# Kernel optimization log

Measured on AMD Instinct MI355X. Metric: run time of the kernel, lower is better.

The kernel has to match this reference:

```python
import jax, jax.numpy as jnp
import numpy as np


def setup_inputs() -> dict:
    key = jax.random.key(0)
    k1, k2 = jax.random.split(key)
    B, T_src, H = 32, 1024, 512
    x = jax.random.normal(k1, (B, T_src, H), dtype=jnp.float32)
    durations = jax.random.randint(k2, (B, T_src), 0, 8, dtype=jnp.int32)
    return {"x": x, "durations": durations}


def reference(x, durations):
    """Length regulator: repeat each source frame x[b, s] durations[b, s] times,
    pad batch to the max expanded length, return (expanded, mel_masks) where
    mel_masks is True at padded positions. Vectorized via cumulative-duration
    searchsorted gather instead of per-batch repeat_interleave.
    x: (B, T_src, H) float, durations: (B, T_src) int.
    """
    B, T_src, H = x.shape
    cum = jnp.cumsum(durations.astype(jnp.int32), axis=1)      # (B, T_src)
    totals = cum[:, -1]                                        # (B,)
    max_len = int(jnp.max(totals))                             # static: concrete inputs
    t = jnp.arange(max_len, dtype=jnp.int32)                   # (T_mel,)
    # src index of output frame t: first s with cum[b, s] > t
    idx = jax.vmap(lambda c: jnp.searchsorted(c, t, side='right'))(cum)  # (B, T_mel)
    idx = jnp.clip(idx, 0, T_src - 1)
    out = jnp.take_along_axis(x, idx[..., None], axis=1)       # (B, T_mel, H)
    mel_masks = t[None, :] >= totals[:, None]                  # (B, T_mel) True = pad
    out = jnp.where(mel_masks[..., None], jnp.zeros((), dtype=x.dtype), out)
    return out, mel_masks
```

## Files before the change

### kernel.cpp

```cpp
#include <hip/hip_runtime.h>


#define B_SZ   32
#define T_SRC  1024
#define H_DIM  512

typedef float f4 __attribute__((ext_vector_type(4)));

__global__ void __launch_bounds__(T_SRC) lr_prep(const int* __restrict__ dur,
                                                 int* __restrict__ cum,
                                                 float* __restrict__ mask,
                                                 int max_len) {
    __shared__ int s[T_SRC];
    const int b   = blockIdx.x;
    const int tid = threadIdx.x;
    s[tid] = dur[b * T_SRC + tid];
    __syncthreads();
#pragma unroll
    for (int off = 1; off < T_SRC; off <<= 1) {
        int v = (tid >= off) ? s[tid - off] : 0;
        __syncthreads();
        s[tid] += v;
        __syncthreads();
    }
    cum[b * T_SRC + tid] = s[tid];
    const int total = s[T_SRC - 1];
    float* mb = mask + (size_t)b * max_len;
    for (int t = tid; t < max_len; t += T_SRC) mb[t] = (t < total) ? 0.0f : 1.0f;
}

__global__ void __launch_bounds__(256) lr_copy(const float* __restrict__ x,
                                               const int* __restrict__ cum,
                                               float* __restrict__ out,
                                               int max_len) {
    const int b    = blockIdx.y;
    const int lane = threadIdx.x & 63;
    const int s    = (blockIdx.x << 2) | (threadIdx.x >> 6);

    const int* cb = cum + b * T_SRC;

    const f4* src = (const f4*)(x + ((size_t)b * T_SRC + s) * H_DIM);
    const f4 v0 = src[lane];
    const f4 v1 = src[lane + 64];

    const int end   = cb[s];
    const int start = s ? cb[s - 1] : 0;

    float* ob = out + (size_t)b * max_len * H_DIM;
    for (int t = start; t < end; ++t) {
        f4* dst = (f4*)(ob + (size_t)t * H_DIM);
        __builtin_nontemporal_store(v0, dst + lane);
        __builtin_nontemporal_store(v1, dst + lane + 64);
    }

    const int total = cb[T_SRC - 1];
    const f4 z = (f4)(0.0f);
    for (int t = total + s; t < max_len; t += T_SRC) {
        f4* dst = (f4*)(ob + (size_t)t * H_DIM);
        __builtin_nontemporal_store(z, dst + lane);
        __builtin_nontemporal_store(z, dst + lane + 64);
    }
}

extern "C" void kernel_launch(void* const* d_in, const int* in_sizes, int n_in,
                              void* d_out, int out_size, void* d_ws, size_t ws_size,
                              hipStream_t stream) {
    const float* x   = (const float*)d_in[0];
    const int*   dur = (const int*)d_in[1];
    float*       out = (float*)d_out;
    int*         cumbuf = (int*)d_ws;

    const int max_len = out_size / (B_SZ * (H_DIM + 1));
    float* mask = out + (size_t)B_SZ * max_len * H_DIM;

    lr_prep<<<B_SZ, T_SRC, 0, stream>>>(dur, cumbuf, mask, max_len);

    dim3 grid(T_SRC / 4, B_SZ);
    lr_copy<<<grid, 256, 0, stream>>>(x, cumbuf, out, max_len);
}
```

Baseline: 293.0 us.

## Fuse cumsum prep into copy kernel with per-block wave-shuffle scan

```diff
diff --git a/kernel.cpp b/kernel.cpp
--- a/kernel.cpp
+++ b/kernel.cpp
@@ -4,61 +4,83 @@
 #define B_SZ   32
 #define T_SRC  1024
 #define H_DIM  512
+#define BLK_PER_B     64
+#define ROWS_PER_BLK  (T_SRC / BLK_PER_B)
+#define ROWS_PER_WAVE (ROWS_PER_BLK / 4)
 
 typedef float f4 __attribute__((ext_vector_type(4)));
+typedef int   i4 __attribute__((ext_vector_type(4)));
 
-__global__ void __launch_bounds__(T_SRC) lr_prep(const int* __restrict__ dur,
-                                                 int* __restrict__ cum,
-                                                 float* __restrict__ mask,
-                                                 int max_len) {
-    __shared__ int s[T_SRC];
-    const int b   = blockIdx.x;
-    const int tid = threadIdx.x;
-    s[tid] = dur[b * T_SRC + tid];
+__global__ void __launch_bounds__(256) lr_fused(const float* __restrict__ x,
+                                                const int* __restrict__ dur,
+                                                float* __restrict__ out,
+                                                float* __restrict__ mask,
+                                                int max_len) {
+    __shared__ int cumsh[T_SRC];
+    __shared__ int wsum[4];
+
+    const int b    = blockIdx.y;
+    const int bx   = blockIdx.x;
+    const int tid  = threadIdx.x;
+    const int lane = tid & 63;
+    const int wid  = tid >> 6;
+
+    const int r0 = bx * ROWS_PER_BLK + wid * ROWS_PER_WAVE;
+    const float* xb = x + (size_t)b * T_SRC * H_DIM;
+    f4 v0[ROWS_PER_WAVE], v1[ROWS_PER_WAVE];
+#pragma unroll
+    for (int i = 0; i < ROWS_PER_WAVE; ++i) {
+        const f4* src = (const f4*)(xb + (size_t)(r0 + i) * H_DIM);
+        v0[i] = src[lane];
+        v1[i] = src[lane + 64];
+    }
+
+    i4 d = ((const i4*)(dur + b * T_SRC))[tid];
+    const int s0 = d.x, s1 = s0 + d.y, s2 = s1 + d.z, s3 = s2 + d.w;
+    int v = s3;
+#pragma unroll
+    for (int off = 1; off < 64; off <<= 1) {
+        int u = __shfl_up(v, off);
+        if (lane >= off) v += u;
+    }
+    if (lane == 63) wsum[wid] = v;
     __syncthreads();
+    int wexcl = 0;
 #pragma unroll
-    for (int off = 1; off < T_SRC; off <<= 1) {
-        int v = (tid >= off) ? s[tid - off] : 0;
-        __syncthreads();
-        s[tid] += v;
-        __syncthreads();
-    }
-    cum[b * T_SRC + tid] = s[tid];
-    const int total = s[T_SRC - 1];
-    float* mb = mask + (size_t)b * max_len;
-    for (int t = tid; t < max_len; t += T_SRC) mb[t] = (t < total) ? 0.0f : 1.0f;
-}
-
-__global__ void __launch_bounds__(256) lr_copy(const float* __restrict__ x,
-                                               const int* __restrict__ cum,
-                                               float* __restrict__ out,
-                                               int max_len) {
-    const int b    = blockIdx.y;
-    const int lane = threadIdx.x & 63;
-    const int s    = (blockIdx.x << 2) | (threadIdx.x >> 6);
-
-    const int* cb = cum + b * T_SRC;
-
-    const f4* src = (const f4*)(x + ((size_t)b * T_SRC + s) * H_DIM);
-    const f4 v0 = src[lane];
-    const f4 v1 = src[lane + 64];
-
-    const int end   = cb[s];
-    const int start = s ? cb[s - 1] : 0;
+    for (int i = 0; i < 4; ++i) if (i < wid) wexcl += wsum[i];
+    const int total = wsum[0] + wsum[1] + wsum[2] + wsum[3];
+    const int gexcl = wexcl + v - s3;
+    cumsh[4 * tid + 0] = gexcl + s0;
+    cumsh[4 * tid + 1] = gexcl + s1;
+    cumsh[4 * tid + 2] = gexcl + s2;
+    cumsh[4 * tid + 3] = gexcl + s3;
+    __syncthreads();
 
     float* ob = out + (size_t)b * max_len * H_DIM;
-    for (int t = start; t < end; ++t) {
-        f4* dst = (f4*)(ob + (size_t)t * H_DIM);
-        __builtin_nontemporal_store(v0, dst + lane);
-        __builtin_nontemporal_store(v1, dst + lane + 64);
+
+#pragma unroll
+    for (int i = 0; i < ROWS_PER_WAVE; ++i) {
+        const int s  = r0 + i;
+        const int en = cumsh[s];
+        const int st = s ? cumsh[s - 1] : 0;
+        for (int t = st; t < en; ++t) {
+            f4* dst = (f4*)(ob + (size_t)t * H_DIM);
+            dst[lane]      = v0[i];
+            dst[lane + 64] = v1[i];
+        }
     }
 
-    const int total = cb[T_SRC - 1];
     const f4 z = (f4)(0.0f);
-    for (int t = total + s; t < max_len; t += T_SRC) {
+    const int wv = (bx << 2) | wid;
+    for (int t = total + wv; t < max_len; t += 4 * BLK_PER_B) {
         f4* dst = (f4*)(ob + (size_t)t * H_DIM);
-        __builtin_nontemporal_store(z, dst + lane);
-        __builtin_nontemporal_store(z, dst + lane + 64);
+        dst[lane]      = z;
+        dst[lane + 64] = z;
+    }
+
+    float* mb = mask + (size_t)b * max_len;
+    for (int t = (bx << 8) | tid; t < max_len; t += BLK_PER_B * 256) {
+        mb[t] = (t < total) ? 0.0f : 1.0f;
     }
 }
 
@@ -68,13 +90,10 @@
     const float* x   = (const float*)d_in[0];
     const int*   dur = (const int*)d_in[1];
     float*       out = (float*)d_out;
-    int*         cumbuf = (int*)d_ws;
 
     const int max_len = out_size / (B_SZ * (H_DIM + 1));
     float* mask = out + (size_t)B_SZ * max_len * H_DIM;
 
-    lr_prep<<<B_SZ, T_SRC, 0, stream>>>(dur, cumbuf, mask, max_len);
-
-    dim3 grid(T_SRC / 4, B_SZ);
-    lr_copy<<<grid, 256, 0, stream>>>(x, cumbuf, out, max_len);
+    dim3 grid(BLK_PER_B, B_SZ);
+    lr_fused<<<grid, 256, 0, stream>>>(x, dur, out, mask, max_len);
 }
```

Measured after the change: 297.2 us. No clear change (+1.4%).
